# Performance work log

Measured on AMD Instinct MI355X. Metric: run time of the kernel, lower is better.

Reference implementation:

```python
import jax, jax.numpy as jnp
import numpy as np

BATCH = 4
N_MELS, T_LEN, PATCH = 128, 512, 16
D_MODEL, D_INNER, D_STATE, DT_RANK, D_CONV = 512, 1024, 16, 32, 4
DEPTH, N_CLASSES = 4, 10


def _silu(x):
    return x * jax.nn.sigmoid(x)


def _ln(x, w, b):
    m = x.mean(-1, keepdims=True)
    v = ((x - m) ** 2).mean(-1, keepdims=True)
    return (x - m) * jax.lax.rsqrt(v + 1e-5) * w + b


def _causal_conv(x, w, b):
    # x: (B, L, D); w: (D, K) depthwise causal conv (mamba conv1d)
    K, L = w.shape[-1], x.shape[1]
    xp = jnp.pad(x, ((0, 0), (K - 1, 0), (0, 0)))
    y = sum(xp[:, k:k + L, :] * w[:, k] for k in range(K))
    return y + b


def _ssm(xc, conv_w, conv_b, xproj_w, dtproj_w, dtproj_b, A_log, Dp):
    # One directional selective scan (mamba S6).
    u = _silu(_causal_conv(xc, conv_w, conv_b))              # (B,L,Di)
    xdbl = jnp.einsum('bld,ed->ble', u, xproj_w)             # (B,L,dt_rank+2S)
    dtr, Bm, Cm = jnp.split(xdbl, [DT_RANK, DT_RANK + D_STATE], axis=-1)
    dt = jax.nn.softplus(jnp.einsum('blr,dr->bld', dtr, dtproj_w) + dtproj_b)
    A = -jnp.exp(A_log)                                      # (Di,S)
    dA = jnp.exp(dt[..., None] * A)                          # (B,L,Di,S)
    dBu = (dt * u)[..., None] * Bm[:, :, None, :]            # (B,L,Di,S)

    def comb(e1, e2):
        a1, b1 = e1
        a2, b2 = e2
        return a1 * a2, a2 * b1 + b2

    _, h = jax.lax.associative_scan(comb, (dA, dBu), axis=1)  # parallel linear recurrence
    return jnp.einsum('blds,bls->bld', h, Cm) + u * Dp


def _forward(x, patch_w, patch_b, in_proj_w, conv_w_f, conv_b_f, conv_w_b, conv_b_b,
             xproj_w_f, xproj_w_b, dtproj_w_f, dtproj_b_f, dtproj_w_b, dtproj_b_b,
             A_log_f, A_log_b, D_f, D_b, out_proj_w, norm_w, norm_b,
             normf_w, normf_b, ln_w, ln_b, fc1_w, fc1_b, fc2_w, fc2_b):
    B = x.shape[0]
    # Patch embed: conv with kernel == stride -> reshape + einsum
    xp = x.reshape(B, 1, N_MELS // PATCH, PATCH, T_LEN // PATCH, PATCH)
    tok = jnp.einsum('bchpwq,dcpq->bhwd', xp, patch_w) + patch_b
    h = tok.reshape(B, -1, D_MODEL)                           # (B, 256, D)
    for i in range(DEPTH):
        xn = _ln(h, norm_w[i], norm_b[i])
        xz = jnp.einsum('bld,ed->ble', xn, in_proj_w[i])
        xc, z = jnp.split(xz, 2, axis=-1)
        y_f = _ssm(xc, conv_w_f[i], conv_b_f[i], xproj_w_f[i],
                   dtproj_w_f[i], dtproj_b_f[i], A_log_f[i], D_f[i])
        y_b = jnp.flip(_ssm(jnp.flip(xc, 1), conv_w_b[i], conv_b_b[i], xproj_w_b[i],
                            dtproj_w_b[i], dtproj_b_b[i], A_log_b[i], D_b[i]), 1)
        y = (y_f + y_b) * _silu(z)                            # bimamba v2: fwd + flipped bwd, gated
        h = h + jnp.einsum('bld,ed->ble', y, out_proj_w[i])
    h = _ln(h, normf_w, normf_b)
    feat = h.mean(axis=1)                                     # pooled features (B, D)
    c = _ln(feat, ln_w, ln_b)
    c = jnp.maximum(c @ fc1_w.T + fc1_b, 0.0)
    return c @ fc2_w.T + fc2_b


def setup_inputs() -> dict:
    ks = iter(jax.random.split(jax.random.key(0), 64))

    def rn(shape, s=0.02):
        return jax.random.normal(next(ks), shape, jnp.float32) * s

    inp = {}
    inp['x'] = jax.random.normal(next(ks), (BATCH, 1, N_MELS, T_LEN), jnp.float32)
    inp['patch_w'] = rn((D_MODEL, 1, PATCH, PATCH))
    inp['patch_b'] = jnp.zeros((D_MODEL,), jnp.float32)
    inp['in_proj_w'] = rn((DEPTH, 2 * D_INNER, D_MODEL))
    A_init = jnp.log(jnp.tile(jnp.arange(1, D_STATE + 1, dtype=jnp.float32), (DEPTH, D_INNER, 1)))
    for sfx in ('f', 'b'):
        inp[f'conv_w_{sfx}'] = rn((DEPTH, D_INNER, D_CONV), 0.2)
        inp[f'conv_b_{sfx}'] = jnp.zeros((DEPTH, D_INNER), jnp.float32)
        inp[f'xproj_w_{sfx}'] = rn((DEPTH, DT_RANK + 2 * D_STATE, D_INNER))
        inp[f'dtproj_w_{sfx}'] = rn((DEPTH, D_INNER, DT_RANK), 0.1)
        inp[f'dtproj_b_{sfx}'] = jnp.full((DEPTH, D_INNER), -4.6, jnp.float32)  # softplus -> dt ~ 0.01
        inp[f'A_log_{sfx}'] = A_init
        inp[f'D_{sfx}'] = jnp.ones((DEPTH, D_INNER), jnp.float32)
    inp['out_proj_w'] = rn((DEPTH, D_MODEL, D_INNER))
    inp['norm_w'] = jnp.ones((DEPTH, D_MODEL), jnp.float32)
    inp['norm_b'] = jnp.zeros((DEPTH, D_MODEL), jnp.float32)
    inp['normf_w'] = jnp.ones((D_MODEL,), jnp.float32)
    inp['normf_b'] = jnp.zeros((D_MODEL,), jnp.float32)
    inp['ln_w'] = jnp.ones((D_MODEL,), jnp.float32)
    inp['ln_b'] = jnp.zeros((D_MODEL,), jnp.float32)
    inp['fc1_w'] = rn((512, D_MODEL))
    inp['fc1_b'] = jnp.zeros((512,), jnp.float32)
    inp['fc2_w'] = rn((N_CLASSES, 512))
    inp['fc2_b'] = jnp.zeros((N_CLASSES,), jnp.float32)
    return inp


def reference(x, patch_w, patch_b, in_proj_w, conv_w_f, conv_b_f, conv_w_b, conv_b_b,
              xproj_w_f, xproj_w_b, dtproj_w_f, dtproj_b_f, dtproj_w_b, dtproj_b_b,
              A_log_f, A_log_b, D_f, D_b, out_proj_w, norm_w, norm_b,
              normf_w, normf_b, ln_w, ln_b, fc1_w, fc1_b, fc2_w, fc2_b):
    return _forward(x, patch_w, patch_b, in_proj_w, conv_w_f, conv_b_f, conv_w_b, conv_b_b,
                    xproj_w_f, xproj_w_b, dtproj_w_f, dtproj_b_f, dtproj_w_b, dtproj_b_b,
                    A_log_f, A_log_b, D_f, D_b, out_proj_w, norm_w, norm_b,
                    normf_w, normf_b, ln_w, ln_b, fc1_w, fc1_b, fc2_w, fc2_b)
```

## Files before the change

### kernel.cpp

```cpp
#include <hip/hip_runtime.h>


#define BB 4
#define LL 256
#define DM 512
#define DI 1024
#define LDST 40

typedef unsigned short u16;
typedef unsigned int u32;
typedef __attribute__((ext_vector_type(8))) short s8v;
typedef __attribute__((ext_vector_type(4))) float f4v;

__device__ __forceinline__ float silu_f(float x){ return x/(1.f+__expf(-x)); }
__device__ __forceinline__ float b2f(u16 u){
  union { u32 i; float f; } v; v.i = ((u32)u) << 16; return v.f;
}
__device__ __forceinline__ void b2x2(u32 w, float& lo, float& hi){
  union { u32 i; float f; } a, b;
  a.i = w << 16; b.i = w & 0xffff0000u;
  lo = a.f; hi = b.f;
}
__device__ __forceinline__ u16 f2bf(float f){
  union { float f; u32 u; } v; v.f = f;
  u32 r = (v.u + 0x7fffu + ((v.u >> 16) & 1u)) >> 16;
  return (u16)r;
}
__device__ __forceinline__ void split8(const float* f, s8v& hi, s8v& lo){
#pragma unroll
  for (int j = 0; j < 8; ++j){
    u16 h = f2bf(f[j]);
    float hf = b2f(h);
    hi[j] = (short)h;
    lo[j] = (short)f2bf(f[j] - hf);
  }
}

__device__ __forceinline__ float row_sum16(float p){
  union { float f; int i; } v, r;
  v.f = p;
  r.i = __builtin_amdgcn_update_dpp(0, v.i, 0x111, 0xF, 0xF, true); v.f += r.f;
  r.i = __builtin_amdgcn_update_dpp(0, v.i, 0x112, 0xF, 0xF, true); v.f += r.f;
  r.i = __builtin_amdgcn_update_dpp(0, v.i, 0x114, 0xF, 0xF, true); v.f += r.f;
  r.i = __builtin_amdgcn_update_dpp(0, v.i, 0x118, 0xF, 0xF, true); v.f += r.f;
  return v.f;
}

__device__ __forceinline__ void block_reduce2(float& a, float& b, float* sc, int nw){
  int lane = threadIdx.x & 63, wid = threadIdx.x >> 6;
#pragma unroll
  for (int o = 32; o > 0; o >>= 1){
    a += __shfl_down(a, o, 64);
    b += __shfl_down(b, o, 64);
  }
  if (lane == 0){ sc[wid*2] = a; sc[wid*2+1] = b; }
  __syncthreads();
  float ta = 0.f, tb = 0.f;
  for (int i = 0; i < nw; ++i){ ta += sc[i*2]; tb += sc[i*2+1]; }
  a = ta; b = tb;
}

__global__ __launch_bounds__(256) void convert_w_all(const float* __restrict__ inW,
    const float* __restrict__ outW, const float* __restrict__ xwF,
    const float* __restrict__ xwB, const float* __restrict__ dtwF,
    const float* __restrict__ dtwB, u16* __restrict__ inHi, u16* __restrict__ inLo,
    u16* __restrict__ outHi, u16* __restrict__ outLo, u16* __restrict__ xwHi,
    u16* __restrict__ xwLo, u16* __restrict__ dtwHi, u16* __restrict__ dtwLo){
  int lay = blockIdx.y;
  int idx = blockIdx.x*256 + threadIdx.x;
  const float4* src; ushort4* dh; ushort4* dl;
  if (idx < 262144){
    src = (const float4*)(inW + (size_t)lay*1048576) + idx;
    dh = (ushort4*)(inHi + (size_t)lay*1048576) + idx;
    dl = (ushort4*)(inLo + (size_t)lay*1048576) + idx;
  } else if (idx < 393216){
    int j = idx - 262144;
    src = (const float4*)(outW + (size_t)lay*524288) + j;
    dh = (ushort4*)(outHi + (size_t)lay*524288) + j;
    dl = (ushort4*)(outLo + (size_t)lay*524288) + j;
  } else if (idx < 409600){
    int j = idx - 393216;
    src = (const float4*)(xwF + (size_t)lay*65536) + j;
    dh = (ushort4*)(xwHi + (size_t)lay*131072) + j;
    dl = (ushort4*)(xwLo + (size_t)lay*131072) + j;
  } else if (idx < 425984){
    int j = idx - 409600;
    src = (const float4*)(xwB + (size_t)lay*65536) + j;
    dh = (ushort4*)(xwHi + (size_t)lay*131072 + 65536) + j;
    dl = (ushort4*)(xwLo + (size_t)lay*131072 + 65536) + j;
  } else if (idx < 434176){
    int j = idx - 425984;
    src = (const float4*)(dtwF + (size_t)lay*32768) + j;
    dh = (ushort4*)(dtwHi + (size_t)lay*65536) + j;
    dl = (ushort4*)(dtwLo + (size_t)lay*65536) + j;
  } else {
    int j = idx - 434176;
    src = (const float4*)(dtwB + (size_t)lay*32768) + j;
    dh = (ushort4*)(dtwHi + (size_t)lay*65536 + 32768) + j;
    dl = (ushort4*)(dtwLo + (size_t)lay*65536 + 32768) + j;
  }
  float4 v = *src;
  ushort4 h, l;
  h.x = f2bf(v.x); l.x = f2bf(v.x - b2f(h.x));
  h.y = f2bf(v.y); l.y = f2bf(v.y - b2f(h.y));
  h.z = f2bf(v.z); l.z = f2bf(v.z - b2f(h.z));
  h.w = f2bf(v.w); l.w = f2bf(v.w - b2f(h.w));
  *dh = h; *dl = l;
}

__global__ __launch_bounds__(256) void patch_embed(const float* __restrict__ x,
    const float* __restrict__ pw, const float* __restrict__ pb, float* __restrict__ h){
  __shared__ float xs[8*256];
  int blk = blockIdx.x;
  int b = blk >> 6, ph = (blk >> 3) & 7, pg = (blk >> 1) & 3, dh = blk & 1;
  int t = threadIdx.x;
  for (int idx = t; idx < 2048; idx += 256){
    int j = idx >> 8, pix = idx & 255, p = pix >> 4, q = pix & 15;
    xs[idx] = x[(size_t)(b*128 + ph*16 + p)*512 + pg*128 + j*16 + q];
  }
  __syncthreads();
  int d = dh*256 + t;
  float acc[8] = {};
  const float* wr = pw + (size_t)d*256;
  for (int i = 0; i < 256; i += 8){
    float4 w0 = *(const float4*)(wr + i);
    float4 w1 = *(const float4*)(wr + i + 4);
    float wf[8] = {w0.x,w0.y,w0.z,w0.w,w1.x,w1.y,w1.z,w1.w};
#pragma unroll
    for (int j = 0; j < 8; ++j){
#pragma unroll
      for (int jj = 0; jj < 8; ++jj)
        acc[j] = fmaf(xs[j*256 + i + jj], wf[jj], acc[j]);
    }
  }
  float bias = pb[d];
#pragma unroll
  for (int j = 0; j < 8; ++j)
    h[(size_t)(b*256 + ph*32 + pg*8 + j)*512 + d] = acc[j] + bias;
}

__global__ __launch_bounds__(256) void prep_ln(const float* __restrict__ x,
    const float* __restrict__ w, const float* __restrict__ bias, int wOff,
    u16* __restrict__ hiO, u16* __restrict__ loO, float* __restrict__ xdblZ){
  __shared__ float sc[8];
  int row = blockIdx.x, t = threadIdx.x;
  if (t < 128) xdblZ[(size_t)row*128 + t] = 0.f;
  const float* xr = x + (size_t)row*DM;
  float v0 = xr[t], v1 = xr[t + 256];
  float s = v0 + v1, ss = v0*v0 + v1*v1;
  block_reduce2(s, ss, sc, 4);
  float mean = s * (1.f/512.f);
  float var = ss * (1.f/512.f) - mean*mean;
  float inv = rsqrtf(var + 1e-5f);
  float o0 = (v0 - mean)*inv*w[wOff + t]       + bias[wOff + t];
  float o1 = (v1 - mean)*inv*w[wOff + t + 256] + bias[wOff + t + 256];
  u16 h0 = f2bf(o0), h1 = f2bf(o1);
  hiO[(size_t)row*DM + t]       = h0;
  hiO[(size_t)row*DM + t + 256] = h1;
  loO[(size_t)row*DM + t]       = f2bf(o0 - b2f(h0));
  loO[(size_t)row*DM + t + 256] = f2bf(o1 - b2f(h1));
}

__global__ __launch_bounds__(256) void prep_gate(const float* __restrict__ ybuf,
    const float* __restrict__ xz, u16* __restrict__ gHi, u16* __restrict__ gLo){
  int row = blockIdx.x, t = threadIdx.x;
  int c = t*4;
  float4 yf = *(const float4*)(ybuf + (size_t)row*DI + c);
  float4 yb = *(const float4*)(ybuf + 1048576 + (size_t)row*DI + c);
  float4 zv = *(const float4*)(xz + (size_t)row*2048 + 1024 + c);
  float g0 = (yf.x + yb.x)*silu_f(zv.x);
  float g1 = (yf.y + yb.y)*silu_f(zv.y);
  float g2 = (yf.z + yb.z)*silu_f(zv.z);
  float g3 = (yf.w + yb.w)*silu_f(zv.w);
  ushort4 h, l;
  h.x = f2bf(g0); l.x = f2bf(g0 - b2f(h.x));
  h.y = f2bf(g1); l.y = f2bf(g1 - b2f(h.y));
  h.z = f2bf(g2); l.z = f2bf(g2 - b2f(h.z));
  h.w = f2bf(g3); l.w = f2bf(g3 - b2f(h.w));
  *(ushort4*)(gHi + (size_t)row*DI + c) = h;
  *(ushort4*)(gLo + (size_t)row*DI + c) = l;
}

__global__ __launch_bounds__(256) void gemm_bf16(const u16* __restrict__ Ahi_g,
    const u16* __restrict__ Alo_g, int As, const u16* __restrict__ Bhi_g,
    const u16* __restrict__ Blo_g, int Bs, float* __restrict__ C, int Cs,
    int K, int addFlag){
  __shared__ __align__(16) u16 Ah[64*LDST], Al[64*LDST], Bh[64*LDST], Bl[64*LDST];
  int bm = blockIdx.y*64, bn = blockIdx.x*64;
  int t = threadIdx.x;
  int sr = t >> 2, sc8 = (t & 3)*8;
  int lane = t & 63, wv = t >> 6, ml = lane & 15, quad = lane >> 4;
  int mq = wv >> 1, nq = wv & 1;
  f4v acc[2][2] = {};
  for (int k0 = 0; k0 < K; k0 += 32){
    *(uint4*)&Ah[sr*LDST + sc8] = *(const uint4*)(Ahi_g + (size_t)(bm + sr)*As + k0 + sc8);
    *(uint4*)&Al[sr*LDST + sc8] = *(const uint4*)(Alo_g + (size_t)(bm + sr)*As + k0 + sc8);
    *(uint4*)&Bh[sr*LDST + sc8] = *(const uint4*)(Bhi_g + (size_t)(bn + sr)*Bs + k0 + sc8);
    *(uint4*)&Bl[sr*LDST + sc8] = *(const uint4*)(Blo_g + (size_t)(bn + sr)*Bs + k0 + sc8);
    __syncthreads();
    s8v ah[2], al2[2], bh2[2], bl2[2];
#pragma unroll
    for (int mt = 0; mt < 2; ++mt){
      int row = mq*32 + mt*16 + ml;
      ah[mt]  = *(s8v*)&Ah[row*LDST + quad*8];
      al2[mt] = *(s8v*)&Al[row*LDST + quad*8];
    }
#pragma unroll
    for (int nt = 0; nt < 2; ++nt){
      int col = nq*32 + nt*16 + ml;
      bh2[nt] = *(s8v*)&Bh[col*LDST + quad*8];
      bl2[nt] = *(s8v*)&Bl[col*LDST + quad*8];
    }
#pragma unroll
    for (int mt = 0; mt < 2; ++mt)
#pragma unroll
      for (int nt = 0; nt < 2; ++nt){
        acc[mt][nt] = __builtin_amdgcn_mfma_f32_16x16x32_bf16(ah[mt],  bh2[nt], acc[mt][nt], 0, 0, 0);
        acc[mt][nt] = __builtin_amdgcn_mfma_f32_16x16x32_bf16(al2[mt], bh2[nt], acc[mt][nt], 0, 0, 0);
        acc[mt][nt] = __builtin_amdgcn_mfma_f32_16x16x32_bf16(ah[mt],  bl2[nt], acc[mt][nt], 0, 0, 0);
      }
    __syncthreads();
  }
#pragma unroll
  for (int mt = 0; mt < 2; ++mt)
#pragma unroll
    for (int nt = 0; nt < 2; ++nt)
#pragma unroll
      for (int r = 0; r < 4; ++r){
        float* cp = C + (size_t)(bm + mq*32 + mt*16 + quad*4 + r)*Cs +
                    bn + nq*32 + nt*16 + ml;
        if (addFlag) *cp += acc[mt][nt][r];
        else         *cp  = acc[mt][nt][r];
      }
}

__global__ __launch_bounds__(256) void conv_silu_split(const float* __restrict__ xz,
    const float* __restrict__ cwF, const float* __restrict__ cbF,
    const float* __restrict__ cwB, const float* __restrict__ cbB,
    int cwOff, int cbOff, u16* __restrict__ uHi, u16* __restrict__ uLo){
  int blk = blockIdx.x;
  int dir = blk >> 8, rem = blk & 255, b = rem >> 6, lg = rem & 63;
  int l0 = lg*4;
  const float* cw = dir ? cwB : cwF;
  const float* cb = dir ? cbB : cbF;
  int t = threadIdx.x;
  int rbase = (dir*BB + b)*LL;
  for (int dd = 0; dd < 4; ++dd){
    int d = t + dd*256;
    float4 w4 = *(const float4*)(cw + cwOff + d*4);
    float wf[4] = {w4.x, w4.y, w4.z, w4.w};
    float bias = cb[cbOff + d];
#pragma unroll
    for (int r = 0; r < 4; ++r){
      int l = l0 + r;
      float acc = bias;
#pragma unroll
      for (int k = 0; k < 4; ++k){
        int li = l + k - 3;
        if (li >= 0){
          int sl = dir ? (LL-1-li) : li;
          acc = fmaf(xz[(size_t)(b*LL + sl)*2048 + d], wf[k], acc);
        }
      }
      float uval = silu_f(acc);
      u16 h = f2bf(uval);
      uHi[(size_t)(rbase + l)*DI + d] = h;
      uLo[(size_t)(rbase + l)*DI + d] = f2bf(uval - b2f(h));
    }
  }
}

__global__ __launch_bounds__(256) void gemm_xproj_splitk(const u16* __restrict__ uHi,
    const u16* __restrict__ uLo, const u16* __restrict__ xwHi,
    const u16* __restrict__ xwLo, float* __restrict__ xdbl){
  __shared__ __align__(16) u16 Ah[64*LDST], Al[64*LDST], Bh[64*LDST], Bl[64*LDST];
  int bm = blockIdx.y*64;
  int kc = blockIdx.x;
  int dir = bm >> 10;
  const u16* BhG = xwHi + dir*65536;
  const u16* BlG = xwLo + dir*65536;
  int t = threadIdx.x;
  int sr = t >> 2, sc8 = (t & 3)*8;
  int lane = t & 63, wv = t >> 6, ml = lane & 15, quad = lane >> 4;
  int mq = wv >> 1, nq = wv & 1;
  f4v acc[2][2] = {};
  for (int k0 = kc*256; k0 < kc*256 + 256; k0 += 32){
    *(uint4*)&Ah[sr*LDST + sc8] = *(const uint4*)(uHi + (size_t)(bm + sr)*1024 + k0 + sc8);
    *(uint4*)&Al[sr*LDST + sc8] = *(const uint4*)(uLo + (size_t)(bm + sr)*1024 + k0 + sc8);
    *(uint4*)&Bh[sr*LDST + sc8] = *(const uint4*)(BhG + (size_t)sr*1024 + k0 + sc8);
    *(uint4*)&Bl[sr*LDST + sc8] = *(const uint4*)(BlG + (size_t)sr*1024 + k0 + sc8);
    __syncthreads();
    s8v ah[2], al2[2], bh2[2], bl2[2];
#pragma unroll
    for (int mt = 0; mt < 2; ++mt){
      int row = mq*32 + mt*16 + ml;
      ah[mt]  = *(s8v*)&Ah[row*LDST + quad*8];
      al2[mt] = *(s8v*)&Al[row*LDST + quad*8];
    }
#pragma unroll
    for (int nt = 0; nt < 2; ++nt){
      int col = nq*32 + nt*16 + ml;
      bh2[nt] = *(s8v*)&Bh[col*LDST + quad*8];
      bl2[nt] = *(s8v*)&Bl[col*LDST + quad*8];
    }
#pragma unroll
    for (int mt = 0; mt < 2; ++mt)
#pragma unroll
      for (int nt = 0; nt < 2; ++nt){
        acc[mt][nt] = __builtin_amdgcn_mfma_f32_16x16x32_bf16(ah[mt],  bh2[nt], acc[mt][nt], 0, 0, 0);
        acc[mt][nt] = __builtin_amdgcn_mfma_f32_16x16x32_bf16(al2[mt], bh2[nt], acc[mt][nt], 0, 0, 0);
        acc[mt][nt] = __builtin_amdgcn_mfma_f32_16x16x32_bf16(ah[mt],  bl2[nt], acc[mt][nt], 0, 0, 0);
      }
    __syncthreads();
  }
#pragma unroll
  for (int mt = 0; mt < 2; ++mt)
#pragma unroll
    for (int nt = 0; nt < 2; ++nt)
#pragma unroll
      for (int r = 0; r < 4; ++r)
        atomicAdd(xdbl + (size_t)(bm + mq*32 + mt*16 + quad*4 + r)*64 +
                  nq*32 + nt*16 + ml, acc[mt][nt][r]);
}

__global__ __launch_bounds__(256) void gemm_dt(const float* __restrict__ xdbl,
    const u16* __restrict__ dtwHi, const u16* __restrict__ dtwLo,
    const float* __restrict__ dtbF, const float* __restrict__ dtbB, int bOff,
    float* __restrict__ dtOut){
  __shared__ __align__(16) u16 Ah[64*LDST], Al[64*LDST], Bh[64*LDST], Bl[64*LDST];
  int bm = blockIdx.y*64, bn = blockIdx.x*64;
  int dir = bm >> 10;
  const u16* BhG = dtwHi + dir*32768;
  const u16* BlG = dtwLo + dir*32768;
  const float* dtb = dir ? dtbB : dtbF;
  int t = threadIdx.x;
  int sr = t >> 2, sc8 = (t & 3)*8;
  int lane = t & 63, wv = t >> 6, ml = lane & 15, quad = lane >> 4;
  int mq = wv >> 1, nq = wv & 1;
  {
    const float* ap = xdbl + (size_t)(bm + sr)*64 + sc8;
    float4 a0 = *(const float4*)ap;
    float4 a1 = *(const float4*)(ap + 4);
    float af[8] = {a0.x,a0.y,a0.z,a0.w,a1.x,a1.y,a1.z,a1.w};
    s8v hi, lo; split8(af, hi, lo);
    *(s8v*)&Ah[sr*LDST + sc8] = hi;
    *(s8v*)&Al[sr*LDST + sc8] = lo;
  }
  *(uint4*)&Bh[sr*LDST + sc8] = *(const uint4*)(BhG + (size_t)(bn + sr)*32 + sc8);
  *(uint4*)&Bl[sr*LDST + sc8] = *(const uint4*)(BlG + (size_t)(bn + sr)*32 + sc8);
  __syncthreads();
  f4v acc[2][2] = {};
  s8v ah[2], al2[2], bh2[2], bl2[2];
#pragma unroll
  for (int mt = 0; mt < 2; ++mt){
    int row = mq*32 + mt*16 + ml;
    ah[mt]  = *(s8v*)&Ah[row*LDST + quad*8];
    al2[mt] = *(s8v*)&Al[row*LDST + quad*8];
  }
#pragma unroll
  for (int nt = 0; nt < 2; ++nt){
    int col = nq*32 + nt*16 + ml;
    bh2[nt] = *(s8v*)&Bh[col*LDST + quad*8];
    bl2[nt] = *(s8v*)&Bl[col*LDST + quad*8];
  }
#pragma unroll
  for (int mt = 0; mt < 2; ++mt)
#pragma unroll
    for (int nt = 0; nt < 2; ++nt){
      acc[mt][nt] = __builtin_amdgcn_mfma_f32_16x16x32_bf16(ah[mt],  bh2[nt], acc[mt][nt], 0, 0, 0);
      acc[mt][nt] = __builtin_amdgcn_mfma_f32_16x16x32_bf16(al2[mt], bh2[nt], acc[mt][nt], 0, 0, 0);
      acc[mt][nt] = __builtin_amdgcn_mfma_f32_16x16x32_bf16(ah[mt],  bl2[nt], acc[mt][nt], 0, 0, 0);
    }
#pragma unroll
  for (int mt = 0; mt < 2; ++mt)
#pragma unroll
    for (int nt = 0; nt < 2; ++nt){
      int col = bn + nq*32 + nt*16 + ml;
      float bias = dtb[bOff + col];
#pragma unroll
      for (int r = 0; r < 4; ++r){
        int row = bm + mq*32 + mt*16 + quad*4 + r;
        float sv = acc[mt][nt][r] + bias;
        dtOut[(size_t)row*1024 + col] = (sv > 15.f) ? sv : log1pf(__expf(sv));
      }
    }
}

__global__ __launch_bounds__(256) void scan_coal(const float* __restrict__ dt,
    const u16* __restrict__ uHi, const u16* __restrict__ uLo,
    const float* __restrict__ xd,
    const float* __restrict__ AlogF, const float* __restrict__ AlogB,
    const float* __restrict__ DF, const float* __restrict__ DB,
    int aOff, int dOff, float* __restrict__ y){
  __shared__ __align__(16) float dtuT[16][516];
  __shared__ __align__(16) float BCT[16][516];
  __shared__ __align__(16) float ytile[128][16];
  int blk = blockIdx.x;
  int dir = blk >> 8, b = (blk >> 6) & 3, dg = blk & 63;
  int t = threadIdx.x;
  int rbase = (dir*BB + b)*LL;
  const float* Alog = dir ? AlogB : AlogF;
  const float* Dpt  = dir ? DB : DF;
  {
    int q = t & 3, lb = t >> 2;
    for (int pass = 0; pass < 4; ++pass){
      int l = pass*64 + lb;
      size_t base = (size_t)(rbase + l)*DI + dg*16 + q*4;
      float4 dv = *(const float4*)(dt + base);
      uint2 uh = *(const uint2*)(uHi + base);
      uint2 ul = *(const uint2*)(uLo + base);
      float h0,h1,h2,h3,l0f,l1f,l2f,l3f;
      b2x2(uh.x, h0, h1); b2x2(uh.y, h2, h3);
      b2x2(ul.x, l0f, l1f); b2x2(ul.y, l2f, l3f);
      float2 p0 = {dv.x, h0 + l0f}, p1 = {dv.y, h1 + l1f};
      float2 p2 = {dv.z, h2 + l2f}, p3 = {dv.w, h3 + l3f};
      *(float2*)&dtuT[q*4+0][l*2] = p0;
      *(float2*)&dtuT[q*4+1][l*2] = p1;
      *(float2*)&dtuT[q*4+2][l*2] = p2;
      *(float2*)&dtuT[q*4+3][l*2] = p3;
    }
  }
  {
    int h8 = t & 7, lb = t >> 3;
    for (int pass = 0; pass < 8; ++pass){
      int l = pass*32 + lb;
      float4 v = *(const float4*)(xd + (size_t)(rbase + l)*64 + 32 + h8*4);
      if (h8 < 4){
        int s0 = h8*4;
        BCT[s0+0][l*2] = v.x; BCT[s0+1][l*2] = v.y;
        BCT[s0+2][l*2] = v.z; BCT[s0+3][l*2] = v.w;
      } else {
        int s0 = (h8-4)*4;
        BCT[s0+0][l*2+1] = v.x; BCT[s0+1][l*2+1] = v.y;
        BCT[s0+2][l*2+1] = v.z; BCT[s0+3][l*2+1] = v.w;
      }
    }
  }
  int s = t & 15, dl = t >> 4;
  float Av = -__expf(Alog[aOff + dg*256 + t]);
  float Dp = Dpt[dOff + dg*16 + dl];
  __syncthreads();
  float h = 0.f;
  for (int half = 0; half < 2; ++half){
    for (int l0 = half*128; l0 < half*128 + 128; l0 += 4){
      float4 du01 = *(const float4*)&dtuT[dl][l0*2];
      float4 du23 = *(const float4*)&dtuT[dl][l0*2 + 4];
      float4 bc01 = *(const float4*)&BCT[s][l0*2];
      float4 bc23 = *(const float4*)&BCT[s][l0*2 + 4];
      float dtv[4] = {du01.x, du01.z, du23.x, du23.z};
      float uv[4]  = {du01.y, du01.w, du23.y, du23.w};
      float Bv[4]  = {bc01.x, bc01.z, bc23.x, bc23.z};
      float Cv[4]  = {bc01.y, bc01.w, bc23.y, bc23.w};
#pragma unroll
      for (int i = 0; i < 4; ++i){
        float a = __expf(dtv[i] * Av);
        h = fmaf(a, h, dtv[i]*uv[i]*Bv[i]);
        float p = h * Cv[i];
        float sum = row_sum16(p);
        if (s == 15){
          int lr = (l0 + i) & 127;
          ytile[lr][dl] = fmaf(uv[i], Dp, sum);
        }
      }
    }
    __syncthreads();
    {
      int d4 = t & 3, lh = t >> 2;
      for (int pass = 0; pass < 2; ++pass){
        int lr = pass*64 + lh;
        int l = half*128 + lr;
        int lo = dir ? (255 - l) : l;
        float4 vv = *(const float4*)&ytile[lr][d4*4];
        *(float4*)(y + (size_t)(rbase + lo)*DI + dg*16 + d4*4) = vv;
      }
    }
    __syncthreads();
  }
}

__global__ __launch_bounds__(256) void ln_kernel(const float* __restrict__ x,
    const float* __restrict__ w, const float* __restrict__ bias,
    float* __restrict__ y){
  __shared__ float sc[8];
  int row = blockIdx.x, t = threadIdx.x;
  const float* xr = x + (size_t)row*DM;
  float v0 = xr[t], v1 = xr[t + 256];
  float s = v0 + v1, ss = v0*v0 + v1*v1;
  block_reduce2(s, ss, sc, 4);
  float mean = s * (1.f/512.f);
  float var = ss * (1.f/512.f) - mean*mean;
  float inv = rsqrtf(var + 1e-5f);
  float* yr = y + (size_t)row*DM;
  yr[t]       = (v0 - mean)*inv*w[t]       + bias[t];
  yr[t + 256] = (v1 - mean)*inv*w[t + 256] + bias[t + 256];
}

__global__ __launch_bounds__(256) void pool_kernel(const float* __restrict__ hn,
    float* __restrict__ feat){
  __shared__ float part[4][64];
  int b = blockIdx.x >> 3, dg = blockIdx.x & 7;
  int t = threadIdx.x, dl = t & 63, lq = t >> 6;
  const float* p = hn + (size_t)(b*256 + lq*64)*512 + dg*64 + dl;
  float s = 0.f;
#pragma unroll 4
  for (int i = 0; i < 64; ++i) s += p[(size_t)i*512];
  part[lq][dl] = s;
  __syncthreads();
  if (t < 64)
    feat[b*512 + dg*64 + t] =
        (part[0][t] + part[1][t] + part[2][t] + part[3][t]) * (1.f/256.f);
}

__global__ __launch_bounds__(512) void head_kernel(const float* __restrict__ feat,
    const float* __restrict__ lnw, const float* __restrict__ lnb,
    const float* __restrict__ fc1w, const float* __restrict__ fc1b,
    const float* __restrict__ fc2w, const float* __restrict__ fc2b,
    float* __restrict__ out){
  __shared__ float sc[16];
  __shared__ float cbuf[512];
  __shared__ float rbuf[512];
  int b = blockIdx.x, t = threadIdx.x;
  float v = feat[b*512 + t];
  float s = v, ss = v*v;
  block_reduce2(s, ss, sc, 8);
  float mean = s * (1.f/512.f);
  float var = ss * (1.f/512.f) - mean*mean;
  float inv = rsqrtf(var + 1e-5f);
  cbuf[t] = (v - mean)*inv*lnw[t] + lnb[t];
  __syncthreads();
  float a = fc1b[t];
  const float* w1 = fc1w + (size_t)t*512;
  for (int i = 0; i < 512; i += 8){
    float4 w0 = *(const float4*)(w1 + i);
    float4 w4 = *(const float4*)(w1 + i + 4);
    float wf[8] = {w0.x,w0.y,w0.z,w0.w,w4.x,w4.y,w4.z,w4.w};
#pragma unroll
    for (int j = 0; j < 8; ++j) a = fmaf(cbuf[i + j], wf[j], a);
  }
  rbuf[t] = fmaxf(a, 0.f);
  __syncthreads();
  if (t < 10){
    float a2 = fc2b[t];
    const float* w2 = fc2w + (size_t)t*512;
    for (int i = 0; i < 512; ++i) a2 = fmaf(rbuf[i], w2[i], a2);
    out[b*10 + t] = a2;
  }
}

extern "C" void kernel_launch(void* const* d_in, const int* in_sizes, int n_in,
                              void* d_out, int out_size, void* d_ws, size_t ws_size,
                              hipStream_t stream) {
  (void)in_sizes; (void)n_in; (void)out_size; (void)ws_size;
  const float* x          = (const float*)d_in[0];
  const float* patch_w    = (const float*)d_in[1];
  const float* patch_b    = (const float*)d_in[2];
  const float* in_proj_w  = (const float*)d_in[3];
  const float* conv_w_f   = (const float*)d_in[4];
  const float* conv_b_f   = (const float*)d_in[5];
  const float* xproj_w_f  = (const float*)d_in[6];
  const float* dtproj_w_f = (const float*)d_in[7];
  const float* dtproj_b_f = (const float*)d_in[8];
  const float* A_log_f    = (const float*)d_in[9];
  const float* D_f        = (const float*)d_in[10];
  const float* conv_w_b   = (const float*)d_in[11];
  const float* conv_b_b   = (const float*)d_in[12];
  const float* xproj_w_b  = (const float*)d_in[13];
  const float* dtproj_w_b = (const float*)d_in[14];
  const float* dtproj_b_b = (const float*)d_in[15];
  const float* A_log_b    = (const float*)d_in[16];
  const float* D_b        = (const float*)d_in[17];
  const float* out_proj_w = (const float*)d_in[18];
  const float* norm_w     = (const float*)d_in[19];
  const float* norm_b     = (const float*)d_in[20];
  const float* normf_w    = (const float*)d_in[21];
  const float* normf_b    = (const float*)d_in[22];
  const float* ln_w       = (const float*)d_in[23];
  const float* ln_b       = (const float*)d_in[24];
  const float* fc1_w      = (const float*)d_in[25];
  const float* fc1_b      = (const float*)d_in[26];
  const float* fc2_w      = (const float*)d_in[27];
  const float* fc2_b      = (const float*)d_in[28];

  float* ws   = (float*)d_ws;
  float* hbuf = ws;
  float* xz   = ws + 524288;
  u16*   uHi  = (u16*)(ws + 2621440);
  u16*   uLo  = (u16*)(ws + 3670016);
  float* xdbl = ws + 4718592;
  float* dtbuf= ws + 4849664;
  float* ybuf = ws + 6946816;
  float* hn   = ws + 9043968;
  float* feat = ws + 11141120;
  u16*   xnHi = (u16*)hn;
  u16*   xnLo = (u16*)(ws + 9306112);
  u16*   gHi  = (u16*)(ws + 2621440);
  u16*   gLo  = (u16*)(ws + 3145728);
  u16*   inHi4 = (u16*)(ws + 11145216);
  u16*   inLo4 = (u16*)(ws + 13242368);
  u16*   outHi4= (u16*)(ws + 15339520);
  u16*   outLo4= (u16*)(ws + 16388096);
  u16*   xwHi4 = (u16*)(ws + 17436672);
  u16*   xwLo4 = (u16*)(ws + 17698816);
  u16*   dtwHi4= (u16*)(ws + 17960960);
  u16*   dtwLo4= (u16*)(ws + 18092032);

  convert_w_all<<<dim3(1728, 4), 256, 0, stream>>>(
      in_proj_w, out_proj_w, xproj_w_f, xproj_w_b, dtproj_w_f, dtproj_w_b,
      inHi4, inLo4, outHi4, outLo4, xwHi4, xwLo4, dtwHi4, dtwLo4);
  patch_embed<<<256, 256, 0, stream>>>(x, patch_w, patch_b, hbuf);
  for (int i = 0; i < 4; ++i){
    prep_ln<<<1024, 256, 0, stream>>>(hbuf, norm_w, norm_b, i*512, xnHi, xnLo, xdbl);
    gemm_bf16<<<dim3(32, 16), 256, 0, stream>>>(
        xnHi, xnLo, 512, inHi4 + (size_t)i*1048576, inLo4 + (size_t)i*1048576,
        512, xz, 2048, 512, 0);
    conv_silu_split<<<512, 256, 0, stream>>>(
        xz, conv_w_f, conv_b_f, conv_w_b, conv_b_b, i*4096, i*1024, uHi, uLo);
    gemm_xproj_splitk<<<dim3(4, 32), 256, 0, stream>>>(
        uHi, uLo, xwHi4 + (size_t)i*131072, xwLo4 + (size_t)i*131072, xdbl);
    gemm_dt<<<dim3(16, 32), 256, 0, stream>>>(
        xdbl, dtwHi4 + (size_t)i*65536, dtwLo4 + (size_t)i*65536,
        dtproj_b_f, dtproj_b_b, i*1024, dtbuf);
    scan_coal<<<512, 256, 0, stream>>>(
        dtbuf, uHi, uLo, xdbl, A_log_f, A_log_b, D_f, D_b, i*16384, i*1024, ybuf);
    prep_gate<<<1024, 256, 0, stream>>>(ybuf, xz, gHi, gLo);
    gemm_bf16<<<dim3(8, 16), 256, 0, stream>>>(
        gHi, gLo, 1024, outHi4 + (size_t)i*524288, outLo4 + (size_t)i*524288,
        1024, hbuf, 512, 1024, 1);
  }
  ln_kernel<<<1024, 256, 0, stream>>>(hbuf, normf_w, normf_b, hn);
  pool_kernel<<<32, 256, 0, stream>>>(hn, feat);
  head_kernel<<<4, 512, 0, stream>>>(feat, ln_w, ln_b, fc1_w, fc1_b, fc2_w, fc2_b,
                                     (float*)d_out);
}
```

Measured before the change: 637.4 us.

## Fuse dt projection and softplus into the scan kernel's load phase

```diff
diff --git a/kernel.cpp b/kernel.cpp
--- a/kernel.cpp
+++ b/kernel.cpp
@@ -323,75 +323,14 @@
                   nq*32 + nt*16 + ml, acc[mt][nt][r]);
 }
 
-__global__ __launch_bounds__(256) void gemm_dt(const float* __restrict__ xdbl,
-    const u16* __restrict__ dtwHi, const u16* __restrict__ dtwLo,
-    const float* __restrict__ dtbF, const float* __restrict__ dtbB, int bOff,
-    float* __restrict__ dtOut){
-  __shared__ __align__(16) u16 Ah[64*LDST], Al[64*LDST], Bh[64*LDST], Bl[64*LDST];
-  int bm = blockIdx.y*64, bn = blockIdx.x*64;
-  int dir = bm >> 10;
-  const u16* BhG = dtwHi + dir*32768;
-  const u16* BlG = dtwLo + dir*32768;
-  const float* dtb = dir ? dtbB : dtbF;
-  int t = threadIdx.x;
-  int sr = t >> 2, sc8 = (t & 3)*8;
-  int lane = t & 63, wv = t >> 6, ml = lane & 15, quad = lane >> 4;
-  int mq = wv >> 1, nq = wv & 1;
-  {
-    const float* ap = xdbl + (size_t)(bm + sr)*64 + sc8;
-    float4 a0 = *(const float4*)ap;
-    float4 a1 = *(const float4*)(ap + 4);
-    float af[8] = {a0.x,a0.y,a0.z,a0.w,a1.x,a1.y,a1.z,a1.w};
-    s8v hi, lo; split8(af, hi, lo);
-    *(s8v*)&Ah[sr*LDST + sc8] = hi;
-    *(s8v*)&Al[sr*LDST + sc8] = lo;
-  }
-  *(uint4*)&Bh[sr*LDST + sc8] = *(const uint4*)(BhG + (size_t)(bn + sr)*32 + sc8);
-  *(uint4*)&Bl[sr*LDST + sc8] = *(const uint4*)(BlG + (size_t)(bn + sr)*32 + sc8);
-  __syncthreads();
-  f4v acc[2][2] = {};
-  s8v ah[2], al2[2], bh2[2], bl2[2];
-#pragma unroll
-  for (int mt = 0; mt < 2; ++mt){
-    int row = mq*32 + mt*16 + ml;
-    ah[mt]  = *(s8v*)&Ah[row*LDST + quad*8];
-    al2[mt] = *(s8v*)&Al[row*LDST + quad*8];
-  }
-#pragma unroll
-  for (int nt = 0; nt < 2; ++nt){
-    int col = nq*32 + nt*16 + ml;
-    bh2[nt] = *(s8v*)&Bh[col*LDST + quad*8];
-    bl2[nt] = *(s8v*)&Bl[col*LDST + quad*8];
-  }
-#pragma unroll
-  for (int mt = 0; mt < 2; ++mt)
-#pragma unroll
-    for (int nt = 0; nt < 2; ++nt){
-      acc[mt][nt] = __builtin_amdgcn_mfma_f32_16x16x32_bf16(ah[mt],  bh2[nt], acc[mt][nt], 0, 0, 0);
-      acc[mt][nt] = __builtin_amdgcn_mfma_f32_16x16x32_bf16(al2[mt], bh2[nt], acc[mt][nt], 0, 0, 0);
-      acc[mt][nt] = __builtin_amdgcn_mfma_f32_16x16x32_bf16(ah[mt],  bl2[nt], acc[mt][nt], 0, 0, 0);
-    }
-#pragma unroll
-  for (int mt = 0; mt < 2; ++mt)
-#pragma unroll
-    for (int nt = 0; nt < 2; ++nt){
-      int col = bn + nq*32 + nt*16 + ml;
-      float bias = dtb[bOff + col];
-#pragma unroll
-      for (int r = 0; r < 4; ++r){
-        int row = bm + mq*32 + mt*16 + quad*4 + r;
-        float sv = acc[mt][nt][r] + bias;
-        dtOut[(size_t)row*1024 + col] = (sv > 15.f) ? sv : log1pf(__expf(sv));
-      }
-    }
-}
-
-__global__ __launch_bounds__(256) void scan_coal(const float* __restrict__ dt,
+__global__ __launch_bounds__(256) void scan_coal(
     const u16* __restrict__ uHi, const u16* __restrict__ uLo,
     const float* __restrict__ xd,
+    const float* __restrict__ dtwF, const float* __restrict__ dtwB,
+    const float* __restrict__ dtbF, const float* __restrict__ dtbB,
     const float* __restrict__ AlogF, const float* __restrict__ AlogB,
     const float* __restrict__ DF, const float* __restrict__ DB,
-    int aOff, int dOff, float* __restrict__ y){
+    int dtwOff, int bOff, int aOff, int dOff, float* __restrict__ y){
   __shared__ __align__(16) float dtuT[16][516];
   __shared__ __align__(16) float BCT[16][516];
   __shared__ __align__(16) float ytile[128][16];
@@ -402,22 +341,33 @@
   const float* Alog = dir ? AlogB : AlogF;
   const float* Dpt  = dir ? DB : DF;
   {
-    int q = t & 3, lb = t >> 2;
-    for (int pass = 0; pass < 4; ++pass){
-      int l = pass*64 + lb;
-      size_t base = (size_t)(rbase + l)*DI + dg*16 + q*4;
-      float4 dv = *(const float4*)(dt + base);
-      uint2 uh = *(const uint2*)(uHi + base);
-      uint2 ul = *(const uint2*)(uLo + base);
-      float h0,h1,h2,h3,l0f,l1f,l2f,l3f;
-      b2x2(uh.x, h0, h1); b2x2(uh.y, h2, h3);
-      b2x2(ul.x, l0f, l1f); b2x2(ul.y, l2f, l3f);
-      float2 p0 = {dv.x, h0 + l0f}, p1 = {dv.y, h1 + l1f};
-      float2 p2 = {dv.z, h2 + l2f}, p3 = {dv.w, h3 + l3f};
-      *(float2*)&dtuT[q*4+0][l*2] = p0;
-      *(float2*)&dtuT[q*4+1][l*2] = p1;
-      *(float2*)&dtuT[q*4+2][l*2] = p2;
-      *(float2*)&dtuT[q*4+3][l*2] = p3;
+    int d_local = t & 15, lc = t >> 4;
+    int d = dg*16 + d_local;
+    const float* dtw = (dir ? dtwB : dtwF) + dtwOff + (size_t)d*32;
+    float wreg[32];
+#pragma unroll
+    for (int k = 0; k < 32; k += 4){
+      float4 w4 = *(const float4*)(dtw + k);
+      wreg[k] = w4.x; wreg[k+1] = w4.y; wreg[k+2] = w4.z; wreg[k+3] = w4.w;
+    }
+    float bias = (dir ? dtbB : dtbF)[bOff + d];
+    for (int i = 0; i < 16; ++i){
+      int l = lc*16 + i;
+      const float* xr = xd + (size_t)(rbase + l)*64;
+      float acc = bias;
+#pragma unroll
+      for (int k = 0; k < 32; k += 4){
+        float4 v = *(const float4*)(xr + k);
+        acc = fmaf(v.x, wreg[k],   acc);
+        acc = fmaf(v.y, wreg[k+1], acc);
+        acc = fmaf(v.z, wreg[k+2], acc);
+        acc = fmaf(v.w, wreg[k+3], acc);
+      }
+      float dtv = (acc > 15.f) ? acc : log1pf(__expf(acc));
+      size_t ub = (size_t)(rbase + l)*DI + d;
+      float uval = b2f(uHi[ub]) + b2f(uLo[ub]);
+      float2 pr = {dtv, uval};
+      *(float2*)&dtuT[d_local][l*2] = pr;
     }
   }
   {
@@ -587,7 +537,6 @@
   u16*   uHi  = (u16*)(ws + 2621440);
   u16*   uLo  = (u16*)(ws + 3670016);
   float* xdbl = ws + 4718592;
-  float* dtbuf= ws + 4849664;
   float* ybuf = ws + 6946816;
   float* hn   = ws + 9043968;
   float* feat = ws + 11141120;
@@ -617,11 +566,9 @@
         xz, conv_w_f, conv_b_f, conv_w_b, conv_b_b, i*4096, i*1024, uHi, uLo);
     gemm_xproj_splitk<<<dim3(4, 32), 256, 0, stream>>>(
         uHi, uLo, xwHi4 + (size_t)i*131072, xwLo4 + (size_t)i*131072, xdbl);
-    gemm_dt<<<dim3(16, 32), 256, 0, stream>>>(
-        xdbl, dtwHi4 + (size_t)i*65536, dtwLo4 + (size_t)i*65536,
-        dtproj_b_f, dtproj_b_b, i*1024, dtbuf);
     scan_coal<<<512, 256, 0, stream>>>(
-        dtbuf, uHi, uLo, xdbl, A_log_f, A_log_b, D_f, D_b, i*16384, i*1024, ybuf);
+        uHi, uLo, xdbl, dtproj_w_f, dtproj_w_b, dtproj_b_f, dtproj_b_b,
+        A_log_f, A_log_b, D_f, D_b, i*32768, i*1024, i*16384, i*1024, ybuf);
     prep_gate<<<1024, 256, 0, stream>>>(ybuf, xz, gHi, gLo);
     gemm_bf16<<<dim3(8, 16), 256, 0, stream>>>(
         gHi, gLo, 1024, outHi4 + (size_t)i*524288, outLo4 + (size_t)i*524288,
```

Result: no change. 624.9 us (-2.0%).
